# Optimization experiments

Measured on AMD Instinct MI355X. Metric: run time of the kernel, lower is better.

## Reference

```python
import jax, jax.numpy as jnp
import numpy as np

NUM_EXPERTS = 64
TOP_K = 2


def setup_inputs() -> dict:
    key = jax.random.key(0)
    k1, k2 = jax.random.split(key)
    B, D, E = 16384, 4096, NUM_EXPERTS
    routing_features = jax.random.normal(k1, (B, D), dtype=jnp.float32)
    # nn.Linear(D, E, bias=False) weight: [E, D], kaiming-uniform-ish init
    bound = 1.0 / np.sqrt(D)
    gate_w = jax.random.uniform(k2, (E, D), dtype=jnp.float32, minval=-bound, maxval=bound)
    return {"routing_features": routing_features, "gate_w": gate_w}


def reference(routing_features, gate_w):
    B = routing_features.shape[0]
    E, K = NUM_EXPERTS, TOP_K
    # linear gate (no bias): [B, E]
    logits = jnp.einsum("bd,ed->be", routing_features, gate_w)
    full_probs = jax.nn.softmax(logits, axis=-1)
    top_k_logits, top_k_indices = jax.lax.top_k(logits, K)  # [B, K]
    top_k_weights = jax.nn.softmax(top_k_logits, axis=-1)
    # load-balance loss: f_i = fraction of (token, slot) assignments to expert i
    tokens_per_expert = jnp.zeros((E,), dtype=jnp.float32).at[top_k_indices.reshape(-1)].add(1.0)
    f = tokens_per_expert / (B * K)
    P = full_probs.mean(axis=0)
    aux_loss = E * jnp.sum(f * P)
    return top_k_weights, top_k_indices, aux_loss
```

## Files before the change

kernel.cpp:

```cpp
#include <hip/hip_runtime.h>
#include <math.h>


typedef __attribute__((ext_vector_type(8))) short bf16x8;
typedef __attribute__((ext_vector_type(4))) float f32x4;

constexpr int B_ROWS  = 16384;
constexpr int D_DIM   = 4096;
constexpr int E_EXP   = 64;
constexpr int TM      = 16;
constexpr int NTHR    = 512;
constexpr int NS      = 16;
constexpr int FLAGCAP = 8192;
constexpr float GAPTHR = 1e-3f;

__device__ __forceinline__ float wave_max64(float v) {
#pragma unroll
  for (int m = 32; m >= 1; m >>= 1) v = fmaxf(v, __shfl_xor(v, m, 64));
  return v;
}
__device__ __forceinline__ float wave_sum64(float v) {
#pragma unroll
  for (int m = 32; m >= 1; m >>= 1) v += __shfl_xor(v, m, 64);
  return v;
}
__device__ __forceinline__ void wave_argmax64(float v, int i, float& mv, int& mi) {
#pragma unroll
  for (int m = 32; m >= 1; m >>= 1) {
    float ov = __shfl_xor(v, m, 64);
    int   oi = __shfl_xor(i, m, 64);
    if (ov > v || (ov == v && oi < i)) { v = ov; i = oi; }
  }
  mv = v; mi = i;
}

__device__ __forceinline__ void split8(const f32x4 a, const f32x4 b, bf16x8& hi, bf16x8& lo) {
  float f[8] = {a[0], a[1], a[2], a[3], b[0], b[1], b[2], b[3]};
#pragma unroll
  for (int i = 0; i < 8; ++i) {
    unsigned int u = __float_as_uint(f[i]);
    hi[i] = (short)(u >> 16);
    float rem = f[i] - __uint_as_float(u & 0xffff0000u);
    lo[i] = (short)(__float_as_uint(rem) >> 16);
  }
}

__global__ __launch_bounds__(NTHR) void wsplit(const float* __restrict__ gw,
                                               char* __restrict__ wsW,
                                               unsigned int* __restrict__ hdr) {
  const int n = blockIdx.x;
  const int t = threadIdx.x;
  if (n == 0 && t < 192) hdr[t] = 0u;
  const int lane = t & 63, h = (t >> 6) & 1, wc = t >> 7;
  const int col = wc * 16 + (lane & 15);
  const int k0  = n * 32 + (lane >> 4) * 8;
  const float* src = gw + (size_t)col * D_DIM + k0;
  union { unsigned short us[8]; uint4 v; } pk;
#pragma unroll
  for (int i = 0; i < 8; ++i) {
    float f = src[i];
    unsigned int u = __float_as_uint(f);
    if (h == 0) {
      pk.us[i] = (unsigned short)(u >> 16);
    } else {
      float rem = f - __uint_as_float(u & 0xffff0000u);
      pk.us[i] = (unsigned short)(__float_as_uint(rem) >> 16);
    }
  }
  *(uint4*)(wsW + (size_t)n * 8192 + (size_t)t * 16) = pk.v;
}

__global__ __launch_bounds__(NTHR) void gemm_router(
    const float* __restrict__ rf, const char* __restrict__ wsW,
    float* __restrict__ out, float* __restrict__ psum,
    unsigned int* __restrict__ cnt, int* __restrict__ flagcnt,
    int* __restrict__ flaglist) {
  __shared__ float lt[TM][E_EXP + 2];
  __shared__ float pcol[E_EXP];
  __shared__ unsigned int scnt[E_EXP];

  const int t = threadIdx.x, lane = t & 63, wv = t >> 6;
  const int row0 = blockIdx.x * TM;

  for (int i = t; i < TM * (E_EXP + 2); i += NTHR) ((float*)lt)[i] = 0.f;
  if (t < E_EXP) { scnt[t] = 0; pcol[t] = 0.f; }
  __syncthreads();

  const float* aptr = rf + (size_t)(row0 + (lane & 15)) * D_DIM
                         + wv * (NS * 32) + (lane >> 4) * 8;
  const char* wbase = wsW + (size_t)(wv * NS) * 8192 + (size_t)lane * 16;

  f32x4 acc[4] = {{0.f,0.f,0.f,0.f},{0.f,0.f,0.f,0.f},{0.f,0.f,0.f,0.f},{0.f,0.f,0.f,0.f}};

  f32x4 aA0, aA1, aB0, aB1;
  bf16x8 wAhi[4], wAlo[4], wBhi[4], wBlo[4];

#define LDA_A(n) { aA0 = *(const f32x4*)(aptr + (n) * 32); \
                   aA1 = *(const f32x4*)(aptr + (n) * 32 + 4); }
#define LDA_B(n) { aB0 = *(const f32x4*)(aptr + (n) * 32); \
                   aB1 = *(const f32x4*)(aptr + (n) * 32 + 4); }
#define LDW_A(n) { const char* wn_ = wbase + (size_t)(n) * 8192; \
    _Pragma("unroll") for (int cb = 0; cb < 4; ++cb) { \
      wAhi[cb] = *(const bf16x8*)(wn_ + cb * 2048); \
      wAlo[cb] = *(const bf16x8*)(wn_ + cb * 2048 + 1024); } }
#define LDW_B(n) { const char* wn_ = wbase + (size_t)(n) * 8192; \
    _Pragma("unroll") for (int cb = 0; cb < 4; ++cb) { \
      wBhi[cb] = *(const bf16x8*)(wn_ + cb * 2048); \
      wBlo[cb] = *(const bf16x8*)(wn_ + cb * 2048 + 1024); } }
#define SBAR __builtin_amdgcn_sched_barrier(0)

  LDA_A(0); LDW_A(0);
  LDA_B(1); LDW_B(1);
  SBAR;
  for (int n = 0; n < NS; n += 2) {
    {
      bf16x8 ahi, alo;
      split8(aA0, aA1, ahi, alo);
      if (n + 2 < NS) LDA_A(n + 2);
      SBAR;
#pragma unroll
      for (int cb = 0; cb < 4; ++cb) {
        acc[cb] = __builtin_amdgcn_mfma_f32_16x16x32_bf16(ahi, wAhi[cb], acc[cb], 0, 0, 0);
        acc[cb] = __builtin_amdgcn_mfma_f32_16x16x32_bf16(alo, wAhi[cb], acc[cb], 0, 0, 0);
        acc[cb] = __builtin_amdgcn_mfma_f32_16x16x32_bf16(ahi, wAlo[cb], acc[cb], 0, 0, 0);
      }
      if (n + 2 < NS) LDW_A(n + 2);
      SBAR;
    }
    {
      bf16x8 ahi, alo;
      split8(aB0, aB1, ahi, alo);
      if (n + 3 < NS) LDA_B(n + 3);
      SBAR;
#pragma unroll
      for (int cb = 0; cb < 4; ++cb) {
        acc[cb] = __builtin_amdgcn_mfma_f32_16x16x32_bf16(ahi, wBhi[cb], acc[cb], 0, 0, 0);
        acc[cb] = __builtin_amdgcn_mfma_f32_16x16x32_bf16(alo, wBhi[cb], acc[cb], 0, 0, 0);
        acc[cb] = __builtin_amdgcn_mfma_f32_16x16x32_bf16(ahi, wBlo[cb], acc[cb], 0, 0, 0);
      }
      if (n + 3 < NS) LDW_B(n + 3);
      SBAR;
    }
  }
#undef LDA_A
#undef LDA_B
#undef LDW_A
#undef LDW_B
#undef SBAR

  {
    const int colb = lane & 15;
    const int rowb = (lane >> 4) * 4;
#pragma unroll
    for (int cb = 0; cb < 4; ++cb)
#pragma unroll
      for (int j = 0; j < 4; ++j)
        atomicAdd(&lt[rowb + j][cb * 16 + colb], acc[cb][j]);
  }
  __syncthreads();

#pragma unroll
  for (int j = 0; j < 2; ++j) {
    const int r = wv * 2 + j;
    const float lg = lt[r][lane];
    const float m  = wave_max64(lg);
    const float p  = __expf(lg - m);
    const float ss = wave_sum64(p);
    atomicAdd(&pcol[lane], p / ss);
    float v1; int i1; wave_argmax64(lg, lane, v1, i1);
    const float lm1 = (lane == i1) ? -INFINITY : lg;
    float v2; int i2; wave_argmax64(lm1, lane, v2, i2);
    const float lm2 = (lane == i2) ? -INFINITY : lm1;
    float v3; int i3; wave_argmax64(lm2, lane, v3, i3);
    if (lane == 0) {
      const float ex = expf(v2 - v1);
      const int row = row0 + r;
      out[row * 2 + 0] = 1.f / (1.f + ex);
      out[row * 2 + 1] = ex / (1.f + ex);
      out[2 * B_ROWS + row * 2 + 0] = (float)i1;
      out[2 * B_ROWS + row * 2 + 1] = (float)i2;
      atomicAdd(&scnt[i1], 1u);
      atomicAdd(&scnt[i2], 1u);
      if (v1 - v2 < GAPTHR || v2 - v3 < GAPTHR) {
        int fi = atomicAdd(flagcnt, 1);
        if (fi < FLAGCAP) flaglist[fi] = row;
      }
    }
  }
  __syncthreads();
  if (t < E_EXP) {
    atomicAdd(&psum[t], pcol[t]);
    const unsigned int c = scnt[t];
    if (c) atomicAdd(&cnt[t], c);
  }
}

__global__ __launch_bounds__(256) void cleanup(
    const float* __restrict__ rf, const float* __restrict__ gw,
    const int* __restrict__ flagcnt, const int* __restrict__ flaglist,
    const float* __restrict__ psum, const unsigned int* __restrict__ cnt,
    float* __restrict__ out) {
  __shared__ double sm[256];
  const int t = threadIdx.x;
  if (blockIdx.x == 0 && t < 64) {
    const float f = (float)cnt[t] / (float)(B_ROWS * 2);
    const float P = psum[t] / (float)B_ROWS;
    float v = wave_sum64(f * P);
    if (t == 0) out[4 * B_ROWS] = (float)E_EXP * v;
  }
  const int nf = min(*flagcnt, FLAGCAP);
  for (int fi = blockIdx.x; fi < nf; fi += gridDim.x) {
    const int row = flaglist[fi];
    const int e = t & 63, seg = t >> 6;
    const float* a = rf + (size_t)row * D_DIM + seg * 1024;
    const float* w = gw + (size_t)e * D_DIM + seg * 1024;
    double p0 = 0.0, p1 = 0.0, p2 = 0.0, p3 = 0.0;
    for (int k = 0; k < 1024; k += 4) {
      p0 = fma((double)a[k + 0], (double)w[k + 0], p0);
      p1 = fma((double)a[k + 1], (double)w[k + 1], p1);
      p2 = fma((double)a[k + 2], (double)w[k + 2], p2);
      p3 = fma((double)a[k + 3], (double)w[k + 3], p3);
    }
    sm[t] = (p0 + p1) + (p2 + p3);
    __syncthreads();
    if (t < 64) {
      const double l = sm[t] + sm[64 + t] + sm[128 + t] + sm[192 + t];
      double v = l; int ii = t;
#pragma unroll
      for (int m = 32; m >= 1; m >>= 1) {
        double ov = __shfl_xor(v, m, 64); int oi = __shfl_xor(ii, m, 64);
        if (ov > v || (ov == v && oi < ii)) { v = ov; ii = oi; }
      }
      const double v1 = v; const int i1 = ii;
      const double lm = (t == i1) ? -1e300 : l;
      v = lm; ii = t;
#pragma unroll
      for (int m = 32; m >= 1; m >>= 1) {
        double ov = __shfl_xor(v, m, 64); int oi = __shfl_xor(ii, m, 64);
        if (ov > v || (ov == v && oi < ii)) { v = ov; ii = oi; }
      }
      const double v2 = v; const int i2 = ii;
      if (t == 0) {
        const double ex = exp(v2 - v1);
        out[row * 2 + 0] = (float)(1.0 / (1.0 + ex));
        out[row * 2 + 1] = (float)(ex / (1.0 + ex));
        out[2 * B_ROWS + row * 2 + 0] = (float)i1;
        out[2 * B_ROWS + row * 2 + 1] = (float)i2;
      }
    }
    __syncthreads();
  }
}

extern "C" void kernel_launch(void* const* d_in, const int* in_sizes, int n_in,
                              void* d_out, int out_size, void* d_ws, size_t ws_size,
                              hipStream_t stream) {
  const float* rf = (const float*)d_in[0];
  const float* gw = (const float*)d_in[1];
  float* out = (float*)d_out;
  float* psum = (float*)d_ws;
  unsigned int* cnt = (unsigned int*)((char*)d_ws + 256);
  int* flagcnt = (int*)((char*)d_ws + 512);
  int* flaglist = (int*)((char*)d_ws + 768);
  char* wsW = (char*)d_ws + 65536;

  wsplit<<<D_DIM / 32, NTHR, 0, stream>>>(gw, wsW, (unsigned int*)d_ws);
  gemm_router<<<B_ROWS / TM, NTHR, 0, stream>>>(rf, wsW, out, psum, cnt,
                                                flagcnt, flaglist);
  cleanup<<<64, 256, 0, stream>>>(rf, gw, flagcnt, flaglist, psum, cnt, out);
}
```

Measured before the change: 216.5 us.

## Split-K GEMM with LDS-staged weights and separate epilogue reduction

Restructures the router GEMM into a split-K kernel. Each block handles 128 rows over a 256-wide K segment, and the bf16 hi/lo weight slice for that segment is staged in LDS via async global-to-LDS copies so the 8 waves share it instead of each reloading weights from global memory. Partial logits are written to a workspace buffer, and a new epilogue kernel sums the 16 partials per row and does the softmax, top-k and counting. This cuts redundant weight traffic and removes the per-block LDS atomic reduction. In exchange it adds a 16×B×E float partial buffer round-trip through memory and an extra kernel launch.

```diff
diff --git a/kernel.cpp b/kernel.cpp
--- a/kernel.cpp
+++ b/kernel.cpp
@@ -8,9 +8,11 @@
 constexpr int B_ROWS  = 16384;
 constexpr int D_DIM   = 4096;
 constexpr int E_EXP   = 64;
-constexpr int TM      = 16;
 constexpr int NTHR    = 512;
-constexpr int NS      = 16;
+constexpr int TM      = 128;
+constexpr int KSEG    = 256;
+constexpr int NSPLIT  = D_DIM / KSEG;
+constexpr int NS      = KSEG / 32;
 constexpr int FLAGCAP = 8192;
 constexpr float GAPTHR = 1e-3f;
 
@@ -32,6 +34,12 @@
     if (ov > v || (ov == v && oi < i)) { v = ov; i = oi; }
   }
   mv = v; mi = i;
+}
+
+__device__ __forceinline__ void async_copy16(void* lds_dst, const void* g_src) {
+  auto g = (const __attribute__((address_space(1))) char*)(g_src);
+  auto l = (__attribute__((address_space(3))) char*)(lds_dst);
+  __builtin_amdgcn_global_load_lds(g, l, 16, 0, 0);
 }
 
 __device__ __forceinline__ void split8(const f32x4 a, const f32x4 b, bf16x8& hi, bf16x8& lo) {
@@ -70,103 +78,92 @@
   *(uint4*)(wsW + (size_t)n * 8192 + (size_t)t * 16) = pk.v;
 }
 
-__global__ __launch_bounds__(NTHR) void gemm_router(
+__global__ __launch_bounds__(NTHR) void gemm_partial(
     const float* __restrict__ rf, const char* __restrict__ wsW,
-    float* __restrict__ out, float* __restrict__ psum,
-    unsigned int* __restrict__ cnt, int* __restrict__ flagcnt,
-    int* __restrict__ flaglist) {
-  __shared__ float lt[TM][E_EXP + 2];
+    float* __restrict__ part) {
+  __shared__ char wlds[NS * 8192] __attribute__((aligned(16)));
+
+  const int t = threadIdx.x, lane = t & 63, wv = t >> 6;
+  const int ks   = blockIdx.x >> 7;
+  const int rb   = blockIdx.x & 127;
+  const int row0 = rb * TM;
+
+  {
+    const char* src = wsW + (size_t)ks * (NS * 8192);
+#pragma unroll
+    for (int i = 0; i < NS; ++i)
+      async_copy16(wlds + i * 8192 + t * 16, src + i * 8192 + t * 16);
+  }
+  __syncthreads();
+
+  const float* aptr = rf + (size_t)(row0 + wv * 16 + (lane & 15)) * D_DIM
+                         + ks * KSEG + (lane >> 4) * 8;
+
+  f32x4 acc[4] = {{0.f,0.f,0.f,0.f},{0.f,0.f,0.f,0.f},{0.f,0.f,0.f,0.f},{0.f,0.f,0.f,0.f}};
+  f32x4 a0[4], a1[4];
+
+#define LDA(s, n) { a0[s] = *(const f32x4*)(aptr + (n) * 32); \
+                    a1[s] = *(const f32x4*)(aptr + (n) * 32 + 4); }
+
+  LDA(0, 0); LDA(1, 1); LDA(2, 2); LDA(3, 3);
+  __builtin_amdgcn_sched_barrier(0);
+
+#pragma unroll
+  for (int n = 0; n < NS; ++n) {
+    const int s = n & 3;
+    bf16x8 ahi, alo;
+    split8(a0[s], a1[s], ahi, alo);
+    if (n + 4 < NS) LDA(s, n + 4);
+    __builtin_amdgcn_sched_barrier(0);
+    const char* wn = wlds + n * 8192 + lane * 16;
+#pragma unroll
+    for (int cb = 0; cb < 4; ++cb) {
+      bf16x8 whi = *(const bf16x8*)(wn + cb * 2048);
+      bf16x8 wlo = *(const bf16x8*)(wn + cb * 2048 + 1024);
+      acc[cb] = __builtin_amdgcn_mfma_f32_16x16x32_bf16(ahi, whi, acc[cb], 0, 0, 0);
+      acc[cb] = __builtin_amdgcn_mfma_f32_16x16x32_bf16(alo, whi, acc[cb], 0, 0, 0);
+      acc[cb] = __builtin_amdgcn_mfma_f32_16x16x32_bf16(ahi, wlo, acc[cb], 0, 0, 0);
+    }
+    __builtin_amdgcn_sched_barrier(0);
+  }
+#undef LDA
+
+  const int colb = lane & 15;
+  const int rowb = (lane >> 4) * 4;
+  float* dst = part + ((size_t)ks * B_ROWS + row0 + wv * 16 + rowb) * E_EXP + colb;
+#pragma unroll
+  for (int cb = 0; cb < 4; ++cb)
+#pragma unroll
+    for (int j = 0; j < 4; ++j)
+      dst[(size_t)j * E_EXP + cb * 16] = acc[cb][j];
+}
+
+__global__ __launch_bounds__(NTHR) void epilogue(
+    const float* __restrict__ part, float* __restrict__ out,
+    float* __restrict__ psum, unsigned int* __restrict__ cnt,
+    int* __restrict__ flagcnt, int* __restrict__ flaglist) {
   __shared__ float pcol[E_EXP];
   __shared__ unsigned int scnt[E_EXP];
 
   const int t = threadIdx.x, lane = t & 63, wv = t >> 6;
-  const int row0 = blockIdx.x * TM;
-
-  for (int i = t; i < TM * (E_EXP + 2); i += NTHR) ((float*)lt)[i] = 0.f;
+  const int row0 = blockIdx.x * 64;
+
   if (t < E_EXP) { scnt[t] = 0; pcol[t] = 0.f; }
   __syncthreads();
 
-  const float* aptr = rf + (size_t)(row0 + (lane & 15)) * D_DIM
-                         + wv * (NS * 32) + (lane >> 4) * 8;
-  const char* wbase = wsW + (size_t)(wv * NS) * 8192 + (size_t)lane * 16;
-
-  f32x4 acc[4] = {{0.f,0.f,0.f,0.f},{0.f,0.f,0.f,0.f},{0.f,0.f,0.f,0.f},{0.f,0.f,0.f,0.f}};
-
-  f32x4 aA0, aA1, aB0, aB1;
-  bf16x8 wAhi[4], wAlo[4], wBhi[4], wBlo[4];
-
-#define LDA_A(n) { aA0 = *(const f32x4*)(aptr + (n) * 32); \
-                   aA1 = *(const f32x4*)(aptr + (n) * 32 + 4); }
-#define LDA_B(n) { aB0 = *(const f32x4*)(aptr + (n) * 32); \
-                   aB1 = *(const f32x4*)(aptr + (n) * 32 + 4); }
-#define LDW_A(n) { const char* wn_ = wbase + (size_t)(n) * 8192; \
-    _Pragma("unroll") for (int cb = 0; cb < 4; ++cb) { \
-      wAhi[cb] = *(const bf16x8*)(wn_ + cb * 2048); \
-      wAlo[cb] = *(const bf16x8*)(wn_ + cb * 2048 + 1024); } }
-#define LDW_B(n) { const char* wn_ = wbase + (size_t)(n) * 8192; \
-    _Pragma("unroll") for (int cb = 0; cb < 4; ++cb) { \
-      wBhi[cb] = *(const bf16x8*)(wn_ + cb * 2048); \
-      wBlo[cb] = *(const bf16x8*)(wn_ + cb * 2048 + 1024); } }
-#define SBAR __builtin_amdgcn_sched_barrier(0)
-
-  LDA_A(0); LDW_A(0);
-  LDA_B(1); LDW_B(1);
-  SBAR;
-  for (int n = 0; n < NS; n += 2) {
-    {
-      bf16x8 ahi, alo;
-      split8(aA0, aA1, ahi, alo);
-      if (n + 2 < NS) LDA_A(n + 2);
-      SBAR;
-#pragma unroll
-      for (int cb = 0; cb < 4; ++cb) {
-        acc[cb] = __builtin_amdgcn_mfma_f32_16x16x32_bf16(ahi, wAhi[cb], acc[cb], 0, 0, 0);
-        acc[cb] = __builtin_amdgcn_mfma_f32_16x16x32_bf16(alo, wAhi[cb], acc[cb], 0, 0, 0);
-        acc[cb] = __builtin_amdgcn_mfma_f32_16x16x32_bf16(ahi, wAlo[cb], acc[cb], 0, 0, 0);
-      }
-      if (n + 2 < NS) LDW_A(n + 2);
-      SBAR;
-    }
-    {
-      bf16x8 ahi, alo;
-      split8(aB0, aB1, ahi, alo);
-      if (n + 3 < NS) LDA_B(n + 3);
-      SBAR;
-#pragma unroll
-      for (int cb = 0; cb < 4; ++cb) {
-        acc[cb] = __builtin_amdgcn_mfma_f32_16x16x32_bf16(ahi, wBhi[cb], acc[cb], 0, 0, 0);
-        acc[cb] = __builtin_amdgcn_mfma_f32_16x16x32_bf16(alo, wBhi[cb], acc[cb], 0, 0, 0);
-        acc[cb] = __builtin_amdgcn_mfma_f32_16x16x32_bf16(ahi, wBlo[cb], acc[cb], 0, 0, 0);
-      }
-      if (n + 3 < NS) LDW_B(n + 3);
-      SBAR;
-    }
-  }
-#undef LDA_A
-#undef LDA_B
-#undef LDW_A
-#undef LDW_B
-#undef SBAR
-
-  {
-    const int colb = lane & 15;
-    const int rowb = (lane >> 4) * 4;
-#pragma unroll
-    for (int cb = 0; cb < 4; ++cb)
-#pragma unroll
-      for (int j = 0; j < 4; ++j)
-        atomicAdd(&lt[rowb + j][cb * 16 + colb], acc[cb][j]);
-  }
-  __syncthreads();
-
-#pragma unroll
-  for (int j = 0; j < 2; ++j) {
-    const int r = wv * 2 + j;
-    const float lg = lt[r][lane];
+#pragma unroll
+  for (int j = 0; j < 8; ++j) {
+    const int row = row0 + wv * 8 + j;
+    float lg = 0.f;
+#pragma unroll
+    for (int s = 0; s < NSPLIT; ++s)
+      lg += part[((size_t)s * B_ROWS + row) * E_EXP + lane];
+
     const float m  = wave_max64(lg);
     const float p  = __expf(lg - m);
     const float ss = wave_sum64(p);
     atomicAdd(&pcol[lane], p / ss);
+
     float v1; int i1; wave_argmax64(lg, lane, v1, i1);
     const float lm1 = (lane == i1) ? -INFINITY : lg;
     float v2; int i2; wave_argmax64(lm1, lane, v2, i2);
@@ -174,7 +171,6 @@
     float v3; int i3; wave_argmax64(lm2, lane, v3, i3);
     if (lane == 0) {
       const float ex = expf(v2 - v1);
-      const int row = row0 + r;
       out[row * 2 + 0] = 1.f / (1.f + ex);
       out[row * 2 + 1] = ex / (1.f + ex);
       out[2 * B_ROWS + row * 2 + 0] = (float)i1;
@@ -262,10 +258,11 @@
   unsigned int* cnt = (unsigned int*)((char*)d_ws + 256);
   int* flagcnt = (int*)((char*)d_ws + 512);
   int* flaglist = (int*)((char*)d_ws + 768);
-  char* wsW = (char*)d_ws + 65536;
+  char* wsW = (char*)d_ws + (1u << 20);
+  float* part = (float*)((char*)d_ws + (2u << 20));
 
   wsplit<<<D_DIM / 32, NTHR, 0, stream>>>(gw, wsW, (unsigned int*)d_ws);
-  gemm_router<<<B_ROWS / TM, NTHR, 0, stream>>>(rf, wsW, out, psum, cnt,
-                                                flagcnt, flaglist);
+  gemm_partial<<<NSPLIT * (B_ROWS / TM), NTHR, 0, stream>>>(rf, wsW, part);
+  epilogue<<<B_ROWS / 64, NTHR, 0, stream>>>(part, out, psum, cnt, flagcnt, flaglist);
   cleanup<<<64, 256, 0, stream>>>(rf, gw, flagcnt, flaglist, psum, cnt, out);
 }
```

Measured after the change: 237.2 us. +9.6%, slower.

## Split K across two waves per block instead of eight, with explicit vmcnt pipelining

Applied to the files above, without the earlier changes.

The router GEMM block shrinks from 8 waves to 2 waves, and each wave now handles a 2048-wide K slice instead of 512. This removes the LDS atomicAdd reduction: wave 0 stores its partials and wave 1 adds its own after a barrier. The double-buffered load loop now uses explicit s_waitcnt vmcnt counts so loads for the next step overlap the MFMAs, and each wave handles 8 rows of the softmax/top-k epilogue instead of 2. Longer per-wave K loops lower the cross-wave reduction cost but reduce per-block parallelism for latency hiding, and correctness depends on the hand-set vmcnt values matching the number of outstanding loads.

```diff
diff --git a/kernel.cpp b/kernel.cpp
--- a/kernel.cpp
+++ b/kernel.cpp
@@ -8,9 +8,9 @@
 constexpr int B_ROWS  = 16384;
 constexpr int D_DIM   = 4096;
 constexpr int E_EXP   = 64;
-constexpr int TM      = 16;
 constexpr int NTHR    = 512;
-constexpr int NS      = 16;
+constexpr int GTHR    = 128;
+constexpr int NS2     = 64;
 constexpr int FLAGCAP = 8192;
 constexpr float GAPTHR = 1e-3f;
 
@@ -70,98 +70,94 @@
   *(uint4*)(wsW + (size_t)n * 8192 + (size_t)t * 16) = pk.v;
 }
 
-__global__ __launch_bounds__(NTHR) void gemm_router(
+__global__ __launch_bounds__(GTHR) void gemm_router(
     const float* __restrict__ rf, const char* __restrict__ wsW,
     float* __restrict__ out, float* __restrict__ psum,
     unsigned int* __restrict__ cnt, int* __restrict__ flagcnt,
     int* __restrict__ flaglist) {
-  __shared__ float lt[TM][E_EXP + 2];
+  __shared__ float lt[16][E_EXP + 1];
   __shared__ float pcol[E_EXP];
   __shared__ unsigned int scnt[E_EXP];
 
   const int t = threadIdx.x, lane = t & 63, wv = t >> 6;
-  const int row0 = blockIdx.x * TM;
-
-  for (int i = t; i < TM * (E_EXP + 2); i += NTHR) ((float*)lt)[i] = 0.f;
+  const int row0 = blockIdx.x * 16;
+
+  const float* aptr = rf + (size_t)(row0 + (lane & 15)) * D_DIM
+                         + wv * (NS2 * 32) + (lane >> 4) * 8;
+  const char* wbase = wsW + (size_t)(wv * NS2) * 8192 + (size_t)lane * 16;
+
+  f32x4 acc[4] = {{0.f,0.f,0.f,0.f},{0.f,0.f,0.f,0.f},{0.f,0.f,0.f,0.f},{0.f,0.f,0.f,0.f}};
+
+  f32x4 aX0, aX1, aY0, aY1;
+  bf16x8 wXhi[4], wXlo[4], wYhi[4], wYlo[4];
+
+#define LDX(n) { const float* ap_ = aptr + (size_t)(n) * 32;                  \
+    aX0 = *(const f32x4*)ap_; aX1 = *(const f32x4*)(ap_ + 4);                 \
+    const char* wp_ = wbase + (size_t)(n) * 8192;                             \
+    _Pragma("unroll") for (int cb = 0; cb < 4; ++cb) {                        \
+      wXhi[cb] = *(const bf16x8*)(wp_ + cb * 2048);                           \
+      wXlo[cb] = *(const bf16x8*)(wp_ + cb * 2048 + 1024); } }
+#define LDY(n) { const float* ap_ = aptr + (size_t)(n) * 32;                  \
+    aY0 = *(const f32x4*)ap_; aY1 = *(const f32x4*)(ap_ + 4);                 \
+    const char* wp_ = wbase + (size_t)(n) * 8192;                             \
+    _Pragma("unroll") for (int cb = 0; cb < 4; ++cb) {                        \
+      wYhi[cb] = *(const bf16x8*)(wp_ + cb * 2048);                           \
+      wYlo[cb] = *(const bf16x8*)(wp_ + cb * 2048 + 1024); } }
+#define MFMA3(AHI, ALO, WH, WL)                                               \
+  _Pragma("unroll") for (int cb = 0; cb < 4; ++cb) {                          \
+    acc[cb] = __builtin_amdgcn_mfma_f32_16x16x32_bf16(AHI, WH[cb], acc[cb], 0, 0, 0); \
+    acc[cb] = __builtin_amdgcn_mfma_f32_16x16x32_bf16(ALO, WH[cb], acc[cb], 0, 0, 0); \
+    acc[cb] = __builtin_amdgcn_mfma_f32_16x16x32_bf16(AHI, WL[cb], acc[cb], 0, 0, 0); }
+
+  LDX(0);
+  LDY(1);
+  for (int n = 0; n < NS2; n += 2) {
+    asm volatile("s_waitcnt vmcnt(10)" ::: "memory");
+    __builtin_amdgcn_sched_barrier(0);
+    {
+      bf16x8 ahi, alo;
+      split8(aX0, aX1, ahi, alo);
+      MFMA3(ahi, alo, wXhi, wXlo);
+    }
+    if (n + 2 < NS2) LDX(n + 2);
+    if (n + 2 < NS2) {
+      asm volatile("s_waitcnt vmcnt(10)" ::: "memory");
+    } else {
+      asm volatile("s_waitcnt vmcnt(0)" ::: "memory");
+    }
+    __builtin_amdgcn_sched_barrier(0);
+    {
+      bf16x8 ahi, alo;
+      split8(aY0, aY1, ahi, alo);
+      MFMA3(ahi, alo, wYhi, wYlo);
+    }
+    if (n + 3 < NS2) LDY(n + 3);
+  }
+#undef LDX
+#undef LDY
+#undef MFMA3
+
+  const int colb = lane & 15;
+  const int rowb = (lane >> 4) * 4;
+  if (wv == 0) {
+#pragma unroll
+    for (int cb = 0; cb < 4; ++cb)
+#pragma unroll
+      for (int j = 0; j < 4; ++j) lt[rowb + j][cb * 16 + colb] = acc[cb][j];
+  }
   if (t < E_EXP) { scnt[t] = 0; pcol[t] = 0.f; }
   __syncthreads();
-
-  const float* aptr = rf + (size_t)(row0 + (lane & 15)) * D_DIM
-                         + wv * (NS * 32) + (lane >> 4) * 8;
-  const char* wbase = wsW + (size_t)(wv * NS) * 8192 + (size_t)lane * 16;
-
-  f32x4 acc[4] = {{0.f,0.f,0.f,0.f},{0.f,0.f,0.f,0.f},{0.f,0.f,0.f,0.f},{0.f,0.f,0.f,0.f}};
-
-  f32x4 aA0, aA1, aB0, aB1;
-  bf16x8 wAhi[4], wAlo[4], wBhi[4], wBlo[4];
-
-#define LDA_A(n) { aA0 = *(const f32x4*)(aptr + (n) * 32); \
-                   aA1 = *(const f32x4*)(aptr + (n) * 32 + 4); }
-#define LDA_B(n) { aB0 = *(const f32x4*)(aptr + (n) * 32); \
-                   aB1 = *(const f32x4*)(aptr + (n) * 32 + 4); }
-#define LDW_A(n) { const char* wn_ = wbase + (size_t)(n) * 8192; \
-    _Pragma("unroll") for (int cb = 0; cb < 4; ++cb) { \
-      wAhi[cb] = *(const bf16x8*)(wn_ + cb * 2048); \
-      wAlo[cb] = *(const bf16x8*)(wn_ + cb * 2048 + 1024); } }
-#define LDW_B(n) { const char* wn_ = wbase + (size_t)(n) * 8192; \
-    _Pragma("unroll") for (int cb = 0; cb < 4; ++cb) { \
-      wBhi[cb] = *(const bf16x8*)(wn_ + cb * 2048); \
-      wBlo[cb] = *(const bf16x8*)(wn_ + cb * 2048 + 1024); } }
-#define SBAR __builtin_amdgcn_sched_barrier(0)
-
-  LDA_A(0); LDW_A(0);
-  LDA_B(1); LDW_B(1);
-  SBAR;
-  for (int n = 0; n < NS; n += 2) {
-    {
-      bf16x8 ahi, alo;
-      split8(aA0, aA1, ahi, alo);
-      if (n + 2 < NS) LDA_A(n + 2);
-      SBAR;
-#pragma unroll
-      for (int cb = 0; cb < 4; ++cb) {
-        acc[cb] = __builtin_amdgcn_mfma_f32_16x16x32_bf16(ahi, wAhi[cb], acc[cb], 0, 0, 0);
-        acc[cb] = __builtin_amdgcn_mfma_f32_16x16x32_bf16(alo, wAhi[cb], acc[cb], 0, 0, 0);
-        acc[cb] = __builtin_amdgcn_mfma_f32_16x16x32_bf16(ahi, wAlo[cb], acc[cb], 0, 0, 0);
-      }
-      if (n + 2 < NS) LDW_A(n + 2);
-      SBAR;
-    }
-    {
-      bf16x8 ahi, alo;
-      split8(aB0, aB1, ahi, alo);
-      if (n + 3 < NS) LDA_B(n + 3);
-      SBAR;
-#pragma unroll
-      for (int cb = 0; cb < 4; ++cb) {
-        acc[cb] = __builtin_amdgcn_mfma_f32_16x16x32_bf16(ahi, wBhi[cb], acc[cb], 0, 0, 0);
-        acc[cb] = __builtin_amdgcn_mfma_f32_16x16x32_bf16(alo, wBhi[cb], acc[cb], 0, 0, 0);
-        acc[cb] = __builtin_amdgcn_mfma_f32_16x16x32_bf16(ahi, wBlo[cb], acc[cb], 0, 0, 0);
-      }
-      if (n + 3 < NS) LDW_B(n + 3);
-      SBAR;
-    }
-  }
-#undef LDA_A
-#undef LDA_B
-#undef LDW_A
-#undef LDW_B
-#undef SBAR
-
-  {
-    const int colb = lane & 15;
-    const int rowb = (lane >> 4) * 4;
+  if (wv == 1) {
 #pragma unroll
     for (int cb = 0; cb < 4; ++cb)
 #pragma unroll
-      for (int j = 0; j < 4; ++j)
-        atomicAdd(&lt[rowb + j][cb * 16 + colb], acc[cb][j]);
+      for (int j = 0; j < 4; ++j) lt[rowb + j][cb * 16 + colb] += acc[cb][j];
   }
   __syncthreads();
 
 #pragma unroll
-  for (int j = 0; j < 2; ++j) {
-    const int r = wv * 2 + j;
+  for (int j = 0; j < 8; ++j) {
+    const int r = wv * 8 + j;
     const float lg = lt[r][lane];
     const float m  = wave_max64(lg);
     const float p  = __expf(lg - m);
@@ -262,10 +258,10 @@
   unsigned int* cnt = (unsigned int*)((char*)d_ws + 256);
   int* flagcnt = (int*)((char*)d_ws + 512);
   int* flaglist = (int*)((char*)d_ws + 768);
-  char* wsW = (char*)d_ws + 65536;
+  char* wsW = (char*)d_ws + (1u << 20);
 
   wsplit<<<D_DIM / 32, NTHR, 0, stream>>>(gw, wsW, (unsigned int*)d_ws);
-  gemm_router<<<B_ROWS / TM, NTHR, 0, stream>>>(rf, wsW, out, psum, cnt,
+  gemm_router<<<B_ROWS / 16, GTHR, 0, stream>>>(rf, wsW, out, psum, cnt,
                                                 flagcnt, flaglist);
   cleanup<<<64, 256, 0, stream>>>(rf, gw, flagcnt, flaglist, psum, cnt, out);
 }
```

Result: slower. 223.7 us (+3.3%).
